# Performance work log

Hardware: AMD Instinct MI355X
Metric: run time of the kernel (lower is better)

The kernel has to match this reference:

```python
import jax, jax.numpy as jnp
import numpy as np

HEADS = 8
DIM_HEAD = 64
SCALE = DIM_HEAD ** -0.5


def setup_inputs() -> dict:
    key = jax.random.key(0)
    k1, k2, k3 = jax.random.split(key, 3)
    B, N, D = 4, 2048, HEADS * DIM_HEAD  # D = inner_dim = 512
    x = jax.random.normal(k1, (B, N, D), dtype=jnp.float32)
    # nn.Linear weights stored transposed vs torch; here we use [in, out]
    w_qkv = jax.random.normal(k2, (D, 3 * D), dtype=jnp.float32) * (D ** -0.5)
    w_out = jax.random.normal(k3, (D, D), dtype=jnp.float32) * (D ** -0.5)
    b_out = jnp.zeros((D,), dtype=jnp.float32)
    return {"x": x, "w_qkv": w_qkv, "w_out": w_out, "b_out": b_out}


def reference(x, w_qkv, w_out, b_out):
    B, N, D = x.shape
    qkv = x @ w_qkv  # [B, N, 3D]
    q, k, v = jnp.split(qkv, 3, axis=-1)

    def to_heads(t):  # b n (h d) -> b h n d
        return t.reshape(B, N, HEADS, DIM_HEAD).transpose(0, 2, 1, 3)

    q, k, v = to_heads(q), to_heads(k), to_heads(v)
    dots = jnp.einsum('bhnd,bhmd->bhnm', q, k) * SCALE  # [B,H,N,N]
    attn = jax.nn.softmax(dots, axis=-1)
    out = jnp.einsum('bhnm,bhmd->bhnd', attn, v)  # [B,H,N,d]
    out = out.transpose(0, 2, 1, 3).reshape(B, N, D)  # b h n d -> b n (h d)
    return out @ w_out + b_out
```

## Files before the change

kernel.cpp:

```cpp
#include <hip/hip_runtime.h>

typedef __bf16 bf16;
typedef __bf16 bf16x8 __attribute__((ext_vector_type(8)));
typedef __bf16 bf16x4 __attribute__((ext_vector_type(4)));
typedef float f32x4 __attribute__((ext_vector_type(4)));
typedef float f32x16 __attribute__((ext_vector_type(16)));

#define MFMA16(a, b, c) __builtin_amdgcn_mfma_f32_16x16x32_bf16(a, b, c, 0, 0, 0)
#define MFMA32(a, b, c) __builtin_amdgcn_mfma_f32_32x32x16_bf16(a, b, c, 0, 0, 0)

#define CS 0.18033688011112042f

__device__ __forceinline__ void load_lds16(const bf16* g, bf16* l) {
    __builtin_amdgcn_global_load_lds(
        (const __attribute__((address_space(1))) unsigned int*)g,
        (__attribute__((address_space(3))) unsigned int*)l, 16, 0, 0);
}

__device__ __forceinline__ bf16x4 shfl_xor32_b64(bf16x4 v) {
    union { bf16x4 b; int i[2]; } u;
    u.b = v;
    u.i[0] = __shfl_xor(u.i[0], 32, 64);
    u.i[1] = __shfl_xor(u.i[1], 32, 64);
    return u.b;
}

__global__ __launch_bounds__(256) void f32_to_bf16_kernel(const float* __restrict__ in,
                                                          bf16* __restrict__ out, int n) {
    int i = (blockIdx.x * 256 + threadIdx.x) * 4;
    if (i < n) {
        float4 v = *(const float4*)&in[i];
        bf16x4 o = {(bf16)v.x, (bf16)v.y, (bf16)v.z, (bf16)v.w};
        *(bf16x4*)&out[i] = o;
    }
}

__global__ __launch_bounds__(256) void transpose_f2b(const float* __restrict__ in,
                                                     bf16* __restrict__ out,
                                                     int R, int C) {
    __shared__ float tile[32][33];
    int tx = threadIdx.x & 31, ty = threadIdx.x >> 5;
    int c0 = blockIdx.x * 32, r0 = blockIdx.y * 32;
#pragma unroll
    for (int i = ty; i < 32; i += 8)
        tile[i][tx] = in[(size_t)(r0 + i) * C + c0 + tx];
    __syncthreads();
#pragma unroll
    for (int i = ty; i < 32; i += 8)
        out[(size_t)(c0 + i) * R + r0 + tx] = (bf16)tile[tx][i];
}

template <int MT, int MODE, typename OutT>
__global__ __launch_bounds__(256, 4) void gemm_bt_kernel(const bf16* __restrict__ A,
                                                         const bf16* __restrict__ Bt,
                                                         const float* __restrict__ bias,
                                                         OutT* __restrict__ C,
                                                         bf16* __restrict__ vt,
                                                         int M, int N, int K) {
    const int BM = MT * 32;
    __shared__ bf16 As[BM * 64];
    __shared__ bf16 Bs[128 * 64];
    int t = threadIdx.x;
    int lane = t & 63, w = t >> 6;
    int wr = w >> 1, wc = w & 1;
    int quad = lane >> 4, r16 = lane & 15;
    int m0 = blockIdx.y * BM, n0 = blockIdx.x * 128;

    const f32x4 fzero = {0.f, 0.f, 0.f, 0.f};
    f32x4 acc[MT][4];
#pragma unroll
    for (int i = 0; i < MT; ++i)
#pragma unroll
        for (int j = 0; j < 4; ++j) acc[i][j] = fzero;

    for (int k0 = 0; k0 < K; k0 += 64) {
        __syncthreads();
#pragma unroll
        for (int ci = t; ci < BM * 8; ci += 256) {
            int row = ci >> 3, cp = ci & 7;
            int cc = cp ^ (row & 7);
            load_lds16(&A[(size_t)(m0 + row) * K + k0 + cc * 8], &As[ci * 8]);
        }
#pragma unroll
        for (int ci = t; ci < 1024; ci += 256) {
            int row = ci >> 3, cp = ci & 7;
            int cc = cp ^ (row & 7);
            load_lds16(&Bt[(size_t)(n0 + row) * K + k0 + cc * 8], &Bs[ci * 8]);
        }
        __syncthreads();
#pragma unroll
        for (int ks = 0; ks < 2; ++ks) {
            bf16x8 af[MT], bfr[4];
            int cp = (ks * 4 + quad) ^ (r16 & 7);
#pragma unroll
            for (int mt = 0; mt < MT; ++mt)
                af[mt] = *(const bf16x8*)&As[(wr * (BM / 2) + mt * 16 + r16) * 64 + cp * 8];
#pragma unroll
            for (int nt = 0; nt < 4; ++nt)
                bfr[nt] = *(const bf16x8*)&Bs[(wc * 64 + nt * 16 + r16) * 64 + cp * 8];
#pragma unroll
            for (int mt = 0; mt < MT; ++mt)
#pragma unroll
                for (int nt = 0; nt < 4; ++nt)
                    acc[mt][nt] = MFMA16(af[mt], bfr[nt], acc[mt][nt]);
        }
    }
#pragma unroll
    for (int mt = 0; mt < MT; ++mt)
#pragma unroll
        for (int nt = 0; nt < 4; ++nt) {
            if (MODE == 1 && n0 >= 1024) {
                int row0 = m0 + wr * (BM / 2) + mt * 16 + quad * 4;
                int col = n0 + wc * 64 + nt * 16 + r16 - 1024;
                bf16x4 ov;
#pragma unroll
                for (int r = 0; r < 4; ++r) ov[r] = (bf16)acc[mt][nt][r];
                *(bf16x4*)&vt[((size_t)((row0 >> 11) * 8 + (col >> 6)) * 64 + (col & 63)) *
                                  2048 + (row0 & 2047)] = ov;
            } else {
#pragma unroll
                for (int r = 0; r < 4; ++r) {
                    int row = m0 + wr * (BM / 2) + mt * 16 + quad * 4 + r;
                    int col = n0 + wc * 64 + nt * 16 + r16;
                    float v = acc[mt][nt][r];
                    if (MODE == 1 && n0 < 512) v *= CS;
                    if (MODE == 2) v += bias[col];
                    C[(size_t)row * N + col] = (OutT)v;
                }
            }
        }
}

__global__ __launch_bounds__(256, 2) void attn_kernel(const bf16* __restrict__ qkv,
                                                      const bf16* __restrict__ vt,
                                                      bf16* __restrict__ out) {
    __shared__ bf16 smem[2][16384];

    int t = threadIdx.x;
    int lane = t & 63, w = t >> 6;
    int h = lane >> 5, q = lane & 31;
    int bh = blockIdx.y, b = bh >> 3, hd = bh & 7;
    int q0 = blockIdx.x * 128 + w * 32;

    bf16x8 qf[4];
    {
        size_t qrow = (size_t)(b * 2048 + q0 + q) * 1536 + hd * 64;
#pragma unroll
        for (int s = 0; s < 4; ++s)
            qf[s] = *(const bf16x8*)&qkv[qrow + s * 16 + h * 8];
    }
    bf16x8 ones;
#pragma unroll
    for (int i = 0; i < 8; ++i) ones[i] = (bf16)1.0f;

    f32x16 o_acc[2], lacc;
#pragma unroll
    for (int i = 0; i < 16; ++i) { o_acc[0][i] = 0.f; o_acc[1][i] = 0.f; lacc[i] = 0.f; }

    auto stage = [&](int kv0, int buf) {
        bf16* Ks = smem[buf];
        bf16* Vs = smem[buf] + 8192;
#pragma unroll
        for (int rdd = 0; rdd < 4; ++rdd) {
            int ci = rdd * 256 + t;
            int row = ci >> 3, cp = ci & 7;
            int cc = cp ^ (row & 7);
            load_lds16(&qkv[(size_t)(b * 2048 + kv0 + row) * 1536 + 512 + hd * 64 + cc * 8],
                       &Ks[ci * 8]);
        }
#pragma unroll
        for (int rdd = 0; rdd < 4; ++rdd) {
            int ci = rdd * 256 + t;
            int row = ci >> 4, cp = ci & 15;
            int cc = (cp & 8) | ((cp & 7) ^ (row & 7));
            load_lds16(&vt[(size_t)(bh * 64 + row) * 2048 + kv0 + cc * 8], &Vs[ci * 8]);
        }
    };

    stage(0, 0);
    for (int it = 0; it < 16; ++it) {
        __syncthreads();
        if (it < 15) stage((it + 1) * 128, (it + 1) & 1);
        const bf16* Ks = smem[it & 1];
        const bf16* Vs = smem[it & 1] + 8192;

#pragma unroll
        for (int sub = 0; sub < 2; ++sub) {
            f32x16 sacc[2];
#pragma unroll
            for (int kb = 0; kb < 2; ++kb)
#pragma unroll
                for (int i = 0; i < 16; ++i) sacc[kb][i] = 0.f;

#pragma unroll
            for (int kb = 0; kb < 2; ++kb) {
                int m = (sub * 2 + kb) * 32 + q;
#pragma unroll
                for (int s = 0; s < 4; ++s) {
                    int cp = (s * 2 + h) ^ (q & 7);
                    bf16x8 kf = *(const bf16x8*)&Ks[m * 64 + cp * 8];
                    sacc[kb] = MFMA32(kf, qf[s], sacc[kb]);
                }
            }

            bf16x8 bfr[4];
#pragma unroll
            for (int kb = 0; kb < 2; ++kb) {
                bf16x4 pk[4];
#pragma unroll
                for (int g = 0; g < 4; ++g)
#pragma unroll
                    for (int i = 0; i < 4; ++i)
                        pk[g][i] = (bf16)exp2f(sacc[kb][4 * g + i]);
#pragma unroll
                for (int wi = 0; wi < 2; ++wi) {
                    bf16x4 plo = pk[2 * wi], phi = pk[2 * wi + 1];
                    bf16x4 xlo = shfl_xor32_b64(plo);
                    bf16x4 xhi = shfl_xor32_b64(phi);
                    bf16x4 lo4 = h ? xhi : plo;
                    bf16x4 hi4 = h ? phi : xlo;
                    bf16x8 bb;
#pragma unroll
                    for (int i = 0; i < 4; ++i) { bb[i] = lo4[i]; bb[4 + i] = hi4[i]; }
                    bfr[kb * 2 + wi] = bb;
                }
            }

#pragma unroll
            for (int j = 0; j < 4; ++j) lacc = MFMA32(ones, bfr[j], lacc);

#pragma unroll
            for (int kstep = 0; kstep < 4; ++kstep)
#pragma unroll
                for (int db = 0; db < 2; ++db) {
                    int d = db * 32 + q;
                    int c = sub * 8 + kstep * 2 + h;
                    int cp = (c & 8) | ((c & 7) ^ (d & 7));
                    bf16x8 vf = *(const bf16x8*)&Vs[d * 128 + cp * 8];
                    o_acc[db] = MFMA32(vf, bfr[kstep], o_acc[db]);
                }
        }
    }

    float linv = 1.f / __shfl(lacc[0], q, 64);

    __syncthreads();
    bf16* Ot = smem[0];
#pragma unroll
    for (int db = 0; db < 2; ++db)
#pragma unroll
        for (int g = 0; g < 4; ++g) {
            bf16x4 ov;
#pragma unroll
            for (int i = 0; i < 4; ++i) ov[i] = (bf16)(o_acc[db][4 * g + i] * linv);
            *(bf16x4*)&Ot[(w * 32 + q) * 72 + db * 32 + g * 8 + h * 4] = ov;
        }
    __syncthreads();
#pragma unroll
    for (int rnd = 0; rnd < 4; ++rnd) {
        int rl = w * 32 + rnd * 8 + (lane >> 3);
        int col = (lane & 7) * 8;
        bf16x8 ov = *(const bf16x8*)&Ot[rl * 72 + col];
        *(bf16x8*)&out[(size_t)(b * 2048 + blockIdx.x * 128 + rl) * 512 + hd * 64 + col] = ov;
    }
}

extern "C" void kernel_launch(void* const* d_in, const int* in_sizes, int n_in,
                              void* d_out, int out_size, void* d_ws, size_t ws_size,
                              hipStream_t stream) {
    const float* x     = (const float*)d_in[0];
    const float* w_qkv = (const float*)d_in[1];
    const float* w_out = (const float*)d_in[2];
    const float* b_out = (const float*)d_in[3];
    float* out = (float*)d_out;

    char* ws = (char*)d_ws;
    size_t off = 0;
    bf16* xb    = (bf16*)(ws + off); off += (size_t)8192 * 512 * 2;
    bf16* wqkvT = (bf16*)(ws + off); off += (size_t)1536 * 512 * 2;
    bf16* woutT = (bf16*)(ws + off); off += (size_t)512 * 512 * 2;
    bf16* qkv   = (bf16*)(ws + off); off += (size_t)8192 * 1536 * 2;
    bf16* vt    = (bf16*)(ws + off); off += (size_t)32 * 64 * 2048 * 2;
    bf16* attn  = (bf16*)(ws + off);

    f32_to_bf16_kernel<<<4096, 256, 0, stream>>>(x, xb, 8192 * 512);
    transpose_f2b<<<dim3(48, 16), 256, 0, stream>>>(w_qkv, wqkvT, 512, 1536);
    transpose_f2b<<<dim3(16, 16), 256, 0, stream>>>(w_out, woutT, 512, 512);
    gemm_bt_kernel<2, 1, bf16><<<dim3(12, 128), 256, 0, stream>>>(
        xb, wqkvT, nullptr, qkv, vt, 8192, 1536, 512);
    attn_kernel<<<dim3(16, 32), 256, 0, stream>>>(qkv, vt, attn);
    gemm_bt_kernel<2, 2, float><<<dim3(4, 128), 256, 0, stream>>>(
        attn, woutT, b_out, out, nullptr, 8192, 512, 512);
}
```

Baseline: 172.8 us.

## Split KV range across warp groups in attention and move V transpose to separate kernel

```diff
diff --git a/kernel.cpp b/kernel.cpp
--- a/kernel.cpp
+++ b/kernel.cpp
@@ -23,6 +23,17 @@
     u.i[0] = __shfl_xor(u.i[0], 32, 64);
     u.i[1] = __shfl_xor(u.i[1], 32, 64);
     return u.b;
+}
+
+__device__ __forceinline__ bf16x8 build_bfrag(bf16x4 plo, bf16x4 phi, int h) {
+    bf16x4 xlo = shfl_xor32_b64(plo);
+    bf16x4 xhi = shfl_xor32_b64(phi);
+    bf16x4 lo4 = h ? xhi : plo;
+    bf16x4 hi4 = h ? phi : xlo;
+    bf16x8 bb;
+#pragma unroll
+    for (int i = 0; i < 4; ++i) { bb[i] = lo4[i]; bb[4 + i] = hi4[i]; }
+    return bb;
 }
 
 __global__ __launch_bounds__(256) void f32_to_bf16_kernel(const float* __restrict__ in,
@@ -50,12 +61,26 @@
         out[(size_t)(c0 + i) * R + r0 + tx] = (bf16)tile[tx][i];
 }
 
+__global__ __launch_bounds__(256) void transpose_v_kernel(const bf16* __restrict__ qkv,
+                                                          bf16* __restrict__ vt) {
+    __shared__ bf16 tile[32][33];
+    int tx = threadIdx.x & 31, ty = threadIdx.x >> 5;
+    int bh = blockIdx.z, b = bh >> 3, h = bh & 7;
+    int n0 = blockIdx.x * 32, d0 = blockIdx.y * 32;
+#pragma unroll
+    for (int i = ty; i < 32; i += 8)
+        tile[i][tx] = qkv[(size_t)(b * 2048 + n0 + i) * 1536 + 1024 + h * 64 + d0 + tx];
+    __syncthreads();
+#pragma unroll
+    for (int i = ty; i < 32; i += 8)
+        vt[(size_t)(bh * 64 + d0 + i) * 2048 + n0 + tx] = tile[tx][i];
+}
+
 template <int MT, int MODE, typename OutT>
 __global__ __launch_bounds__(256, 4) void gemm_bt_kernel(const bf16* __restrict__ A,
                                                          const bf16* __restrict__ Bt,
                                                          const float* __restrict__ bias,
                                                          OutT* __restrict__ C,
-                                                         bf16* __restrict__ vt,
                                                          int M, int N, int K) {
     const int BM = MT * 32;
     __shared__ bf16 As[BM * 64];
@@ -108,46 +133,38 @@
 #pragma unroll
     for (int mt = 0; mt < MT; ++mt)
 #pragma unroll
-        for (int nt = 0; nt < 4; ++nt) {
-            if (MODE == 1 && n0 >= 1024) {
-                int row0 = m0 + wr * (BM / 2) + mt * 16 + quad * 4;
-                int col = n0 + wc * 64 + nt * 16 + r16 - 1024;
-                bf16x4 ov;
-#pragma unroll
-                for (int r = 0; r < 4; ++r) ov[r] = (bf16)acc[mt][nt][r];
-                *(bf16x4*)&vt[((size_t)((row0 >> 11) * 8 + (col >> 6)) * 64 + (col & 63)) *
-                                  2048 + (row0 & 2047)] = ov;
-            } else {
-#pragma unroll
-                for (int r = 0; r < 4; ++r) {
-                    int row = m0 + wr * (BM / 2) + mt * 16 + quad * 4 + r;
-                    int col = n0 + wc * 64 + nt * 16 + r16;
-                    float v = acc[mt][nt][r];
-                    if (MODE == 1 && n0 < 512) v *= CS;
-                    if (MODE == 2) v += bias[col];
-                    C[(size_t)row * N + col] = (OutT)v;
-                }
+        for (int nt = 0; nt < 4; ++nt)
+#pragma unroll
+            for (int r = 0; r < 4; ++r) {
+                int row = m0 + wr * (BM / 2) + mt * 16 + quad * 4 + r;
+                int col = n0 + wc * 64 + nt * 16 + r16;
+                float v = acc[mt][nt][r];
+                if (MODE == 1 && n0 < 512) v *= CS;
+                if (MODE == 2) v += bias[col];
+                C[(size_t)row * N + col] = (OutT)v;
             }
-        }
 }
 
 __global__ __launch_bounds__(256, 2) void attn_kernel(const bf16* __restrict__ qkv,
                                                       const bf16* __restrict__ vt,
                                                       bf16* __restrict__ out) {
-    __shared__ bf16 smem[2][16384];
+    __shared__ bf16 smem[16384];
 
     int t = threadIdx.x;
     int lane = t & 63, w = t >> 6;
     int h = lane >> 5, q = lane & 31;
+    int g = w >> 1, wq = w & 1;
+    int tt = t & 127;
     int bh = blockIdx.y, b = bh >> 3, hd = bh & 7;
-    int q0 = blockIdx.x * 128 + w * 32;
+    int qb = blockIdx.x * 64;
+    int qrow = qb + wq * 32 + q;
 
     bf16x8 qf[4];
     {
-        size_t qrow = (size_t)(b * 2048 + q0 + q) * 1536 + hd * 64;
+        size_t qoff = (size_t)(b * 2048 + qrow) * 1536 + hd * 64;
 #pragma unroll
         for (int s = 0; s < 4; ++s)
-            qf[s] = *(const bf16x8*)&qkv[qrow + s * 16 + h * 8];
+            qf[s] = *(const bf16x8*)&qkv[qoff + s * 16 + h * 8];
     }
     bf16x8 ones;
 #pragma unroll
@@ -157,12 +174,15 @@
 #pragma unroll
     for (int i = 0; i < 16; ++i) { o_acc[0][i] = 0.f; o_acc[1][i] = 0.f; lacc[i] = 0.f; }
 
-    auto stage = [&](int kv0, int buf) {
-        bf16* Ks = smem[buf];
-        bf16* Vs = smem[buf] + 8192;
+    bf16* Ks = &smem[g * 8192];
+    bf16* Vs = Ks + 4096;
+
+    for (int it = 0; it < 16; ++it) {
+        int kv0 = g * 1024 + it * 64;
+        __syncthreads();
 #pragma unroll
         for (int rdd = 0; rdd < 4; ++rdd) {
-            int ci = rdd * 256 + t;
+            int ci = rdd * 128 + tt;
             int row = ci >> 3, cp = ci & 7;
             int cc = cp ^ (row & 7);
             load_lds16(&qkv[(size_t)(b * 2048 + kv0 + row) * 1536 + 512 + hd * 64 + cc * 8],
@@ -170,98 +190,99 @@
         }
 #pragma unroll
         for (int rdd = 0; rdd < 4; ++rdd) {
-            int ci = rdd * 256 + t;
-            int row = ci >> 4, cp = ci & 15;
-            int cc = (cp & 8) | ((cp & 7) ^ (row & 7));
+            int ci = rdd * 128 + tt;
+            int row = ci >> 3, cp = ci & 7;
+            int cc = cp ^ (row & 7);
             load_lds16(&vt[(size_t)(bh * 64 + row) * 2048 + kv0 + cc * 8], &Vs[ci * 8]);
         }
-    };
-
-    stage(0, 0);
-    for (int it = 0; it < 16; ++it) {
         __syncthreads();
-        if (it < 15) stage((it + 1) * 128, (it + 1) & 1);
-        const bf16* Ks = smem[it & 1];
-        const bf16* Vs = smem[it & 1] + 8192;
-
-#pragma unroll
-        for (int sub = 0; sub < 2; ++sub) {
-            f32x16 sacc[2];
-#pragma unroll
-            for (int kb = 0; kb < 2; ++kb)
-#pragma unroll
-                for (int i = 0; i < 16; ++i) sacc[kb][i] = 0.f;
-
-#pragma unroll
-            for (int kb = 0; kb < 2; ++kb) {
-                int m = (sub * 2 + kb) * 32 + q;
-#pragma unroll
-                for (int s = 0; s < 4; ++s) {
-                    int cp = (s * 2 + h) ^ (q & 7);
-                    bf16x8 kf = *(const bf16x8*)&Ks[m * 64 + cp * 8];
-                    sacc[kb] = MFMA32(kf, qf[s], sacc[kb]);
-                }
+
+        f32x16 sacc[2];
+#pragma unroll
+        for (int kb = 0; kb < 2; ++kb)
+#pragma unroll
+            for (int i = 0; i < 16; ++i) sacc[kb][i] = 0.f;
+
+#pragma unroll
+        for (int kb = 0; kb < 2; ++kb) {
+            int m = kb * 32 + q;
+#pragma unroll
+            for (int s = 0; s < 4; ++s) {
+                int cp = (s * 2 + h) ^ (q & 7);
+                bf16x8 kf = *(const bf16x8*)&Ks[m * 64 + cp * 8];
+                sacc[kb] = MFMA32(kf, qf[s], sacc[kb]);
             }
-
-            bf16x8 bfr[4];
-#pragma unroll
-            for (int kb = 0; kb < 2; ++kb) {
-                bf16x4 pk[4];
-#pragma unroll
-                for (int g = 0; g < 4; ++g)
-#pragma unroll
-                    for (int i = 0; i < 4; ++i)
-                        pk[g][i] = (bf16)exp2f(sacc[kb][4 * g + i]);
-#pragma unroll
-                for (int wi = 0; wi < 2; ++wi) {
-                    bf16x4 plo = pk[2 * wi], phi = pk[2 * wi + 1];
-                    bf16x4 xlo = shfl_xor32_b64(plo);
-                    bf16x4 xhi = shfl_xor32_b64(phi);
-                    bf16x4 lo4 = h ? xhi : plo;
-                    bf16x4 hi4 = h ? phi : xlo;
-                    bf16x8 bb;
-#pragma unroll
-                    for (int i = 0; i < 4; ++i) { bb[i] = lo4[i]; bb[4 + i] = hi4[i]; }
-                    bfr[kb * 2 + wi] = bb;
-                }
+        }
+
+        bf16x8 bfr[4];
+#pragma unroll
+        for (int kb = 0; kb < 2; ++kb) {
+            bf16x4 pk[4];
+#pragma unroll
+            for (int g8 = 0; g8 < 4; ++g8)
+#pragma unroll
+                for (int i = 0; i < 4; ++i)
+                    pk[g8][i] = (bf16)exp2f(sacc[kb][4 * g8 + i]);
+#pragma unroll
+            for (int wi = 0; wi < 2; ++wi)
+                bfr[kb * 2 + wi] = build_bfrag(pk[2 * wi], pk[2 * wi + 1], h);
+        }
+
+#pragma unroll
+        for (int j = 0; j < 4; ++j) lacc = MFMA32(ones, bfr[j], lacc);
+
+#pragma unroll
+        for (int kstep = 0; kstep < 4; ++kstep)
+#pragma unroll
+            for (int db = 0; db < 2; ++db) {
+                int d = db * 32 + q;
+                int cp = (kstep * 2 + h) ^ (q & 7);
+                bf16x8 vf = *(const bf16x8*)&Vs[d * 64 + cp * 8];
+                o_acc[db] = MFMA32(vf, bfr[kstep], o_acc[db]);
             }
-
-#pragma unroll
-            for (int j = 0; j < 4; ++j) lacc = MFMA32(ones, bfr[j], lacc);
-
-#pragma unroll
-            for (int kstep = 0; kstep < 4; ++kstep)
-#pragma unroll
-                for (int db = 0; db < 2; ++db) {
-                    int d = db * 32 + q;
-                    int c = sub * 8 + kstep * 2 + h;
-                    int cp = (c & 8) | ((c & 7) ^ (d & 7));
-                    bf16x8 vf = *(const bf16x8*)&Vs[d * 128 + cp * 8];
-                    o_acc[db] = MFMA32(vf, bfr[kstep], o_acc[db]);
-                }
-        }
-    }
-
-    float linv = 1.f / __shfl(lacc[0], q, 64);
-
-    __syncthreads();
-    bf16* Ot = smem[0];
-#pragma unroll
-    for (int db = 0; db < 2; ++db)
-#pragma unroll
-        for (int g = 0; g < 4; ++g) {
-            bf16x4 ov;
-#pragma unroll
-            for (int i = 0; i < 4; ++i) ov[i] = (bf16)(o_acc[db][4 * g + i] * linv);
-            *(bf16x4*)&Ot[(w * 32 + q) * 72 + db * 32 + g * 8 + h * 4] = ov;
-        }
-    __syncthreads();
-#pragma unroll
-    for (int rnd = 0; rnd < 4; ++rnd) {
-        int rl = w * 32 + rnd * 8 + (lane >> 3);
-        int col = (lane & 7) * 8;
-        bf16x8 ov = *(const bf16x8*)&Ot[rl * 72 + col];
-        *(bf16x8*)&out[(size_t)(b * 2048 + blockIdx.x * 128 + rl) * 512 + hd * 64 + col] = ov;
+    }
+
+    float l_own = __shfl(lacc[0], q, 64);
+
+    __syncthreads();
+    float* Of = (float*)smem;
+    float* Lf = (float*)(smem + 8192);
+    bf16*  Ot = smem + 8320;
+
+    if (g == 1) {
+#pragma unroll
+        for (int db = 0; db < 2; ++db)
+#pragma unroll
+            for (int g8 = 0; g8 < 4; ++g8)
+#pragma unroll
+                for (int i = 0; i < 4; ++i)
+                    Of[(wq * 64 + db * 32 + g8 * 8 + h * 4 + i) * 32 + q] =
+                        o_acc[db][g8 * 4 + i];
+        if (h == 0) Lf[wq * 32 + q] = l_own;
+    }
+    __syncthreads();
+    if (g == 0) {
+        float linv = 1.f / (l_own + Lf[wq * 32 + q]);
+#pragma unroll
+        for (int db = 0; db < 2; ++db)
+#pragma unroll
+            for (int g8 = 0; g8 < 4; ++g8) {
+                bf16x4 ov;
+#pragma unroll
+                for (int i = 0; i < 4; ++i)
+                    ov[i] = (bf16)((o_acc[db][g8 * 4 + i] +
+                                    Of[(wq * 64 + db * 32 + g8 * 8 + h * 4 + i) * 32 + q]) *
+                                   linv);
+                *(bf16x4*)&Ot[(wq * 32 + q) * 72 + db * 32 + g8 * 8 + h * 4] = ov;
+            }
+    }
+    __syncthreads();
+#pragma unroll
+    for (int rnd = 0; rnd < 2; ++rnd) {
+        int idx = rnd * 256 + t;
+        int row = idx >> 3, col = (idx & 7) * 8;
+        bf16x8 ov = *(const bf16x8*)&Ot[row * 72 + col];
+        *(bf16x8*)&out[(size_t)(b * 2048 + qb + row) * 512 + hd * 64 + col] = ov;
     }
 }
 
@@ -287,8 +308,9 @@
     transpose_f2b<<<dim3(48, 16), 256, 0, stream>>>(w_qkv, wqkvT, 512, 1536);
     transpose_f2b<<<dim3(16, 16), 256, 0, stream>>>(w_out, woutT, 512, 512);
     gemm_bt_kernel<2, 1, bf16><<<dim3(12, 128), 256, 0, stream>>>(
-        xb, wqkvT, nullptr, qkv, vt, 8192, 1536, 512);
-    attn_kernel<<<dim3(16, 32), 256, 0, stream>>>(qkv, vt, attn);
-    gemm_bt_kernel<2, 2, float><<<dim3(4, 128), 256, 0, stream>>>(
-        attn, woutT, b_out, out, nullptr, 8192, 512, 512);
-}
+        xb, wqkvT, nullptr, qkv, 8192, 1536, 512);
+    transpose_v_kernel<<<dim3(64, 2, 32), 256, 0, stream>>>(qkv, vt);
+    attn_kernel<<<dim3(32, 32), 256, 0, stream>>>(qkv, vt, attn);
+    gemm_bt_kernel<1, 2, float><<<dim3(4, 256), 256, 0, stream>>>(
+        attn, woutT, b_out, out, 8192, 512, 512);
+}
```

Result: slower. 193.5 us (+12.0%).
